# Kernel optimization log

Measured on AMD Instinct MI355X. Metric: run time of the kernel, lower is better.

The kernel has to match this reference:

```python
import jax, jax.numpy as jnp
import numpy as np

N_NODES = 100000
IN_CH, HID_CH, OUT_CH = 128, 256, 128
N_EDGES = 1600000


def setup_inputs() -> dict:
    key = jax.random.key(0)
    ks = jax.random.split(key, 12)
    x = jax.random.normal(ks[0], (N_NODES, IN_CH), dtype=jnp.float32)
    edge_index = jax.random.randint(ks[1], (2, N_EDGES), 0, N_NODES, dtype=jnp.int32)
    s1 = 1.0 / np.sqrt(IN_CH)
    s2 = 1.0 / np.sqrt(HID_CH)
    return {
        "x": x,
        "edge_index": edge_index,
        "eps1": jnp.zeros((), jnp.float32),
        "W1a": jax.random.uniform(ks[2], (IN_CH, HID_CH), jnp.float32, -s1, s1),
        "b1a": jax.random.uniform(ks[3], (HID_CH,), jnp.float32, -s1, s1),
        "W1b": jax.random.uniform(ks[4], (HID_CH, HID_CH), jnp.float32, -s2, s2),
        "b1b": jax.random.uniform(ks[5], (HID_CH,), jnp.float32, -s2, s2),
        "eps2": jnp.zeros((), jnp.float32),
        "W2a": jax.random.uniform(ks[6], (HID_CH, HID_CH), jnp.float32, -s2, s2),
        "b2a": jax.random.uniform(ks[7], (HID_CH,), jnp.float32, -s2, s2),
        "W2b": jax.random.uniform(ks[8], (HID_CH, OUT_CH), jnp.float32, -s2, s2),
        "b2b": jax.random.uniform(ks[9], (OUT_CH,), jnp.float32, -s2, s2),
    }


def _gin_conv(x, src, dst, eps, Wa, ba, Wb, bb):
    # sum-aggregate source features into destinations: [N, d]
    agg = jax.ops.segment_sum(x[src], dst, num_segments=N_NODES)
    h = (1.0 + eps) * x + agg
    h = jax.nn.relu(h @ Wa + ba)
    return h @ Wb + bb


def reference(x, edge_index, eps1, W1a, b1a, W1b, b1b, eps2, W2a, b2a, W2b, b2b):
    src, dst = edge_index[0], edge_index[1]
    h = _gin_conv(x, src, dst, eps1, W1a, b1a, W1b, b1b)
    h = jax.nn.relu(h)
    out = _gin_conv(h, src, dst, eps2, W2a, b2a, W2b, b2b)
    return out
```

## Files before the change

### kernel.cpp

```cpp
#include <hip/hip_runtime.h>

#define N_NODES 100000
#define N_EDGES 1600000
#define NB 782
#define SC_BLK 256

typedef __attribute__((ext_vector_type(8))) short short8;
typedef __attribute__((ext_vector_type(4))) float float4e;

#define GLDS16(g, l)                                                   \
  __builtin_amdgcn_global_load_lds(                                    \
      (const __attribute__((address_space(1))) unsigned int*)(g),      \
      (__attribute__((address_space(3))) unsigned int*)(l), 16, 0, 0)

__device__ __forceinline__ unsigned short f2bf(float f) {
  unsigned u = __float_as_uint(f);
  u += 0x7FFFu + ((u >> 16) & 1u);
  return (unsigned short)(u >> 16);
}
__device__ __forceinline__ float bf2f(unsigned short h) {
  return __uint_as_float(((unsigned)h) << 16);
}

__global__ __launch_bounds__(256) void histA_k(const int* __restrict__ dst,
                                               int* __restrict__ bh, int nE) {
  __shared__ int h[NB];
  const int blk = blockIdx.x, tid = threadIdx.x;
  for (int b = tid; b < NB; b += 256) h[b] = 0;
  __syncthreads();
  const int epb = (nE + SC_BLK - 1) / SC_BLK;
  const int i1 = min(blk * epb + epb, nE);
  for (int i = blk * epb + tid; i < i1; i += 256)
    atomicAdd(&h[dst[i] >> 7], 1);
  __syncthreads();
  for (int b = tid; b < NB; b += 256) bh[b * SC_BLK + blk] = h[b];
}

__global__ __launch_bounds__(256) void scanW_k(int* __restrict__ bh,
                                               int* __restrict__ tot) {
  const int b = blockIdx.x * 4 + (threadIdx.x >> 6);
  const int lane = threadIdx.x & 63;
  if (b >= NB) return;
  const int base = b * SC_BLK + lane * 4;
  int v[4];
#pragma unroll
  for (int j = 0; j < 4; ++j) v[j] = bh[base + j];
  int ls = v[0] + v[1] + v[2] + v[3];
  int x = ls;
  for (int off = 1; off < 64; off <<= 1) {
    int y = __shfl_up(x, off);
    if (lane >= off) x += y;
  }
  int run = x - ls;
#pragma unroll
  for (int j = 0; j < 4; ++j) {
    int t = v[j];
    bh[base + j] = run;
    run += t;
  }
  if (lane == 63) tot[b] = run;
}

__global__ __launch_bounds__(1024) void scanB2_k(const int* __restrict__ tot,
                                                 int* __restrict__ bucketStart) {
  __shared__ int sm[1024];
  const int tid = threadIdx.x;
  int v = (tid < NB) ? tot[tid] : 0;
  sm[tid] = v;
  __syncthreads();
  for (int off = 1; off < 1024; off <<= 1) {
    int t = (tid >= off) ? sm[tid - off] : 0;
    __syncthreads();
    sm[tid] += t;
    __syncthreads();
  }
  if (tid < NB) bucketStart[tid] = sm[tid] - v;
  if (tid == NB - 1) bucketStart[NB] = sm[tid];
}

__global__ __launch_bounds__(256) void scatter2_k(
    const int* __restrict__ src, const int* __restrict__ dst,
    const int* __restrict__ bucketStart, const int* __restrict__ bh,
    unsigned int* __restrict__ packed, int nE) {
  __shared__ int cur[NB];
  const int blk = blockIdx.x, tid = threadIdx.x;
  for (int b = tid; b < NB; b += 256)
    cur[b] = bucketStart[b] + bh[b * SC_BLK + blk];
  __syncthreads();
  const int epb = (nE + SC_BLK - 1) / SC_BLK;
  const int i1 = min(blk * epb + epb, nE);
  for (int i = blk * epb + tid; i < i1; i += 256) {
    int d = dst[i];
    int s = src[i];
    int p = atomicAdd(&cur[d >> 7], 1);
    packed[p] = ((unsigned)s << 7) | (unsigned)(d & 127);
  }
}

__global__ __launch_bounds__(256) void fillB_k(
    const int* __restrict__ bucketStart, const unsigned int* __restrict__ packed,
    int* __restrict__ rowEnd, int* __restrict__ sortedSrc, int nNodes) {
  __shared__ int cnt[128];
  __shared__ int cur[128];
  const int b = blockIdx.x;
  const int tid = threadIdx.x;
  const int s0 = bucketStart[b];
  const int ne = bucketStart[b + 1] - s0;
  if (tid < 128) cnt[tid] = 0;
  __syncthreads();
  for (int i = tid; i < ne; i += 256)
    atomicAdd(&cnt[packed[s0 + i] & 127u], 1);
  __syncthreads();
  int v = (tid < 128) ? cnt[tid] : 0;
  for (int off = 1; off < 128; off <<= 1) {
    int t = (tid < 128 && tid >= off) ? cnt[tid - off] : 0;
    __syncthreads();
    if (tid < 128) cnt[tid] += t;
    __syncthreads();
  }
  if (tid < 128) {
    cur[tid] = s0 + cnt[tid] - v;
    int node = b * 128 + tid;
    if (node < nNodes) rowEnd[node] = s0 + cnt[tid];
  }
  __syncthreads();
  for (int i = tid; i < ne; i += 256) {
    unsigned p = packed[s0 + i];
    int idx = atomicAdd(&cur[p & 127u], 1);
    sortedSrc[idx] = (int)(p >> 7);
  }
}

__global__ __launch_bounds__(256) void wprep_k(
    const float* __restrict__ W, unsigned short* __restrict__ th,
    unsigned short* __restrict__ tl, int K, int N) {
  int i = blockIdx.x * blockDim.x + threadIdx.x;
  if (i < K * N) {
    int k = i / N, n = i % N;
    float v = W[i];
    unsigned short h = f2bf(v);
    unsigned short l = f2bf(v - bf2f(h));
    th[(long)n * K + k] = h;
    tl[(long)n * K + k] = l;
  }
}

__global__ __launch_bounds__(256) void xprep_k(const float* __restrict__ x,
                                               unsigned short* __restrict__ xh,
                                               int n) {
  int i = blockIdx.x * blockDim.x + threadIdx.x;
  if (i < n) xh[i] = f2bf(x[i]);
}

template <bool XF32>
__global__ __launch_bounds__(256) void agg_s_k(
    const unsigned short* __restrict__ feat_h, const float* __restrict__ xf,
    const unsigned short* __restrict__ xh, const unsigned short* __restrict__ xl,
    const float* __restrict__ epsp, const int* __restrict__ rowEnd,
    const int* __restrict__ sortedSrc, unsigned short* __restrict__ oh,
    unsigned short* __restrict__ ol, int M, int S, int off) {
  constexpr int V = 2;
  const int lane = threadIdx.x & 63;
  const int w = (int)((blockIdx.x * blockDim.x + threadIdx.x) >> 6);
  if (w >= M) return;
  const int start = w ? rowEnd[w - 1] : 0;
  const int end = rowEnd[w];
  const int c0 = lane * V + off;

  float acc[V] = {};
  int e = start;
  for (; e + 8 <= end; e += 8) {
    int si[8];
#pragma unroll
    for (int q = 0; q < 8; ++q) si[q] = sortedSrc[e + q];
    ushort2 t[8];
#pragma unroll
    for (int q = 0; q < 8; ++q)
      t[q] = *(const ushort2*)(feat_h + (long)si[q] * S + c0);
#pragma unroll
    for (int q = 0; q < 8; ++q) {
      acc[0] += bf2f(t[q].x);
      acc[1] += bf2f(t[q].y);
    }
  }
  for (; e + 4 <= end; e += 4) {
    int s0 = sortedSrc[e + 0];
    int s1 = sortedSrc[e + 1];
    int s2 = sortedSrc[e + 2];
    int s3 = sortedSrc[e + 3];
    ushort2 a = *(const ushort2*)(feat_h + (long)s0 * S + c0);
    ushort2 b = *(const ushort2*)(feat_h + (long)s1 * S + c0);
    ushort2 c = *(const ushort2*)(feat_h + (long)s2 * S + c0);
    ushort2 d = *(const ushort2*)(feat_h + (long)s3 * S + c0);
    acc[0] += bf2f(a.x) + bf2f(b.x) + bf2f(c.x) + bf2f(d.x);
    acc[1] += bf2f(a.y) + bf2f(b.y) + bf2f(c.y) + bf2f(d.y);
  }
  for (; e < end; ++e) {
    ushort2 a = *(const ushort2*)(feat_h + (long)sortedSrc[e] * S + c0);
    acc[0] += bf2f(a.x);
    acc[1] += bf2f(a.y);
  }

  const float s = 1.0f + epsp[0];
  float xv[V];
  if constexpr (XF32) {
#pragma unroll
    for (int v = 0; v < V; ++v) xv[v] = xf[(long)w * S + c0 + v];
  } else {
#pragma unroll
    for (int v = 0; v < V; ++v)
      xv[v] = bf2f(xh[(long)w * S + c0 + v]) + bf2f(xl[(long)w * S + c0 + v]);
  }

  unsigned short hv[V], lv[V];
#pragma unroll
  for (int v = 0; v < V; ++v) {
    float res = fmaf(s, xv[v], acc[v]);
    hv[v] = f2bf(res);
    lv[v] = f2bf(res - bf2f(hv[v]));
  }
  *(ushort2*)&oh[(long)w * S + c0] = make_ushort2(hv[0], hv[1]);
  *(ushort2*)&ol[(long)w * S + c0] = make_ushort2(lv[0], lv[1]);
}

__device__ __forceinline__ short8 lds_rd(const unsigned short* base, int r,
                                         int q) {
  int L = r * 64 + q * 16;
  int P = L ^ (((L >> 7) & 7) << 4);
  return *(const short8*)((const char*)base + P);
}

#define MFMA_BF16 __builtin_amdgcn_mfma_f32_16x16x32_bf16

template <int NY, bool RELU, bool HILO>
__global__ __launch_bounds__(256, 2) void gemm128_k(
    const unsigned short* __restrict__ Ah, const unsigned short* __restrict__ Al,
    const unsigned short* __restrict__ Bth, const unsigned short* __restrict__ Btl,
    const float* __restrict__ bias, float* __restrict__ outf,
    unsigned short* __restrict__ oh, unsigned short* __restrict__ ol,
    int M, int K, int NOUT) {
  __shared__ unsigned short Sm[16384];
  unsigned short* Ash = Sm;
  unsigned short* Asl = Sm + 4096;
  unsigned short* Bsh = Sm + 8192;
  unsigned short* Bsl = Sm + 12288;

  const int tid = threadIdx.x;
  const int lane = tid & 63;
  const int wave = tid >> 6;
  const int l15 = lane & 15;
  const int quad = lane >> 4;
  const int wm = wave >> 1;
  const int wn = wave & 1;

  const int nwg = gridDim.x;
  const int q8 = nwg >> 3, r8 = nwg & 7;
  const int xcd = blockIdx.x & 7, idx = blockIdx.x >> 3;
  const int lin =
      (xcd < r8 ? xcd * (q8 + 1) : r8 * (q8 + 1) + (xcd - r8) * q8) + idx;
  int bx, n0;
  if (NY == 2) {
    bx = lin >> 1;
    n0 = (lin & 1) * 128;
  } else {
    bx = lin;
    n0 = 0;
  }
  const int m0 = bx * 128;

  float4e acc[4][4];
#pragma unroll
  for (int i = 0; i < 4; ++i)
#pragma unroll
    for (int j = 0; j < 4; ++j) acc[i][j] = 0.0f;

  for (int k0 = 0; k0 < K; k0 += 32) {
#pragma unroll
    for (int h = 0; h < 2; ++h) {
      int c = h * 256 + tid;
      int P = c * 16;
      int L = P ^ (((P >> 7) & 7) << 4);
      int r = L >> 6;
      int q = (L >> 4) & 3;
      int ra = min(m0 + r, M - 1);
      long ga = (long)ra * K + k0 + q * 8;
      GLDS16(Ah + ga, &Ash[c * 8]);
      GLDS16(Al + ga, &Asl[c * 8]);
      long gb = (long)(n0 + r) * K + k0 + q * 8;
      GLDS16(Bth + gb, &Bsh[c * 8]);
      GLDS16(Btl + gb, &Bsl[c * 8]);
    }
    __syncthreads();

    short8 ah[4], al[4];
#pragma unroll
    for (int mi = 0; mi < 4; ++mi) {
      ah[mi] = lds_rd(Ash, wm * 64 + mi * 16 + l15, quad);
      al[mi] = lds_rd(Asl, wm * 64 + mi * 16 + l15, quad);
    }
#pragma unroll
    for (int ni = 0; ni < 4; ++ni) {
      short8 bh = lds_rd(Bsh, wn * 64 + ni * 16 + l15, quad);
      short8 bl = lds_rd(Bsl, wn * 64 + ni * 16 + l15, quad);
#pragma unroll
      for (int mi = 0; mi < 4; ++mi) {
        acc[mi][ni] = MFMA_BF16(ah[mi], bh, acc[mi][ni], 0, 0, 0);
        acc[mi][ni] = MFMA_BF16(ah[mi], bl, acc[mi][ni], 0, 0, 0);
        acc[mi][ni] = MFMA_BF16(al[mi], bh, acc[mi][ni], 0, 0, 0);
      }
    }
    __syncthreads();
  }

  if constexpr (HILO) {
#pragma unroll
    for (int pass = 0; pass < 2; ++pass) {
#pragma unroll
      for (int ni = 0; ni < 4; ++ni) {
        int col = wn * 64 + ni * 16 + l15;
        float bj = bias[n0 + col];
#pragma unroll
        for (int mi = 0; mi < 4; ++mi) {
#pragma unroll
          for (int r = 0; r < 4; ++r) {
            int row = wm * 64 + mi * 16 + quad * 4 + r;
            float v = acc[mi][ni][r] + bj;
            if constexpr (RELU) v = fmaxf(v, 0.0f);
            unsigned short hv = f2bf(v);
            unsigned short wv = pass ? f2bf(v - bf2f(hv)) : hv;
            int B = row * 256 + col * 2;
            int SB = B ^ (((row >> 2) & 3) << 5);
            *(unsigned short*)((char*)Sm + SB) = wv;
          }
        }
      }
      __syncthreads();
      unsigned short* dst = pass ? ol : oh;
#pragma unroll
      for (int i = 0; i < 8; ++i) {
        int li = i * 256 + tid;
        int row = li >> 4, chk = li & 15;
        int B = row * 256 + chk * 16;
        int SB = B ^ (((row >> 2) & 3) << 5);
        if (m0 + row < M)
          *(short8*)&dst[(long)(m0 + row) * NOUT + n0 + chk * 8] =
              *(const short8*)((const char*)Sm + SB);
      }
      __syncthreads();
    }
  } else {
#pragma unroll
    for (int ni = 0; ni < 4; ++ni) {
      int col = n0 + wn * 64 + ni * 16 + l15;
      float bj = bias[col];
#pragma unroll
      for (int mi = 0; mi < 4; ++mi) {
        int rbase = m0 + wm * 64 + mi * 16 + quad * 4;
#pragma unroll
        for (int r = 0; r < 4; ++r) {
          int row = rbase + r;
          if (row < M) {
            float v = acc[mi][ni][r] + bj;
            if constexpr (RELU) v = fmaxf(v, 0.0f);
            outf[(long)row * NOUT + col] = v;
          }
        }
      }
    }
  }
}

extern "C" void kernel_launch(void* const* d_in, const int* in_sizes, int n_in,
                              void* d_out, int out_size, void* d_ws, size_t ws_size,
                              hipStream_t stream) {
  const float* x    = (const float*)d_in[0];
  const int*   ei   = (const int*)d_in[1];
  const float* eps1 = (const float*)d_in[2];
  const float* W1a  = (const float*)d_in[3];
  const float* b1a  = (const float*)d_in[4];
  const float* W1b  = (const float*)d_in[5];
  const float* b1b  = (const float*)d_in[6];
  const float* eps2 = (const float*)d_in[7];
  const float* W2a  = (const float*)d_in[8];
  const float* b2a  = (const float*)d_in[9];
  const float* W2b  = (const float*)d_in[10];
  const float* b2b  = (const float*)d_in[11];
  float* out = (float*)d_out;

  const int* srcp = ei;
  const int* dstp = ei + N_EDGES;

  char* ws = (char*)d_ws;
  const size_t SZ = (size_t)N_NODES * 256 * sizeof(float);
  char* P1 = ws;
  char* P2 = ws + SZ;

  unsigned short* C1h = (unsigned short*)P1;
  unsigned short* C1l = C1h + (size_t)N_NODES * 128;
  unsigned short* xh  = C1l + (size_t)N_NODES * 128;
  unsigned short* T1h = (unsigned short*)P2;
  unsigned short* T1l = T1h + (size_t)N_NODES * 256;
  unsigned short* Hh = (unsigned short*)P1;
  unsigned short* Hl = Hh + (size_t)N_NODES * 256;
  unsigned short* C2h = (unsigned short*)P2;
  unsigned short* C2l = C2h + (size_t)N_NODES * 256;
  unsigned short* T2h = (unsigned short*)P1;
  unsigned short* T2l = T2h + (size_t)N_NODES * 256;
  unsigned short* W2bh = (unsigned short*)P2;
  unsigned short* W2bl = W2bh + 128 * 256;

  char* ob = (char*)d_out;
  int* rowEnd    = (int*)(ob + 400 * 1024);
  int* sortedSrc = (int*)(ob + 800 * 1024);
  size_t wofs = 7340032;
  unsigned short* W1ah = (unsigned short*)(ob + wofs);
  unsigned short* W1al = W1ah + 256 * 128;
  unsigned short* W1bh = (unsigned short*)(ob + wofs + 2 * 65536);
  unsigned short* W1bl = W1bh + 256 * 256;
  unsigned short* W2ah = (unsigned short*)(ob + wofs + 2 * 65536 + 2 * 131072);
  unsigned short* W2al = W2ah + 256 * 256;
  unsigned int* packed = (unsigned int*)(ob + 16 * 1024 * 1024);
  int* bucketStart = (int*)(ob + 28 * 1024 * 1024);
  int* bucketTot   = (int*)(ob + 28 * 1024 * 1024 + 8192);
  int* blockHist   = (int*)(ob + 30 * 1024 * 1024);

  dim3 blk(256);
  dim3 gAgg((N_NODES + 3) / 4);
  dim3 gW1((128 * 256 + 255) / 256);
  dim3 gW2((256 * 256 + 255) / 256);
  dim3 gXp((N_NODES * 128 + 255) / 256);
  dim3 gGemm2(((N_NODES + 127) / 128) * 2);
  dim3 gGemm1((N_NODES + 127) / 128);

  histA_k<<<dim3(SC_BLK), blk, 0, stream>>>(dstp, blockHist, N_EDGES);
  scanW_k<<<dim3((NB + 3) / 4), blk, 0, stream>>>(blockHist, bucketTot);
  scanB2_k<<<1, dim3(1024), 0, stream>>>(bucketTot, bucketStart);
  scatter2_k<<<dim3(SC_BLK), blk, 0, stream>>>(srcp, dstp, bucketStart,
                                               blockHist, packed, N_EDGES);
  fillB_k<<<dim3(NB), blk, 0, stream>>>(bucketStart, packed, rowEnd, sortedSrc,
                                        N_NODES);
  xprep_k<<<gXp, blk, 0, stream>>>(x, xh, N_NODES * 128);
  wprep_k<<<gW1, blk, 0, stream>>>(W1a, W1ah, W1al, 128, 256);
  wprep_k<<<gW2, blk, 0, stream>>>(W1b, W1bh, W1bl, 256, 256);
  wprep_k<<<gW2, blk, 0, stream>>>(W2a, W2ah, W2al, 256, 256);

  agg_s_k<true><<<gAgg, blk, 0, stream>>>(
      xh, x, nullptr, nullptr, eps1, rowEnd, sortedSrc, C1h, C1l, N_NODES, 128, 0);
  gemm128_k<2, true, true><<<gGemm2, blk, 0, stream>>>(
      C1h, C1l, W1ah, W1al, b1a, nullptr, T1h, T1l, N_NODES, 128, 256);
  gemm128_k<2, true, true><<<gGemm2, blk, 0, stream>>>(
      T1h, T1l, W1bh, W1bl, b1b, nullptr, Hh, Hl, N_NODES, 256, 256);

  agg_s_k<false><<<gAgg, blk, 0, stream>>>(
      Hh, nullptr, Hh, Hl, eps2, rowEnd, sortedSrc, C2h, C2l, N_NODES, 256, 0);
  agg_s_k<false><<<gAgg, blk, 0, stream>>>(
      Hh, nullptr, Hh, Hl, eps2, rowEnd, sortedSrc, C2h, C2l, N_NODES, 256, 128);
  gemm128_k<2, true, true><<<gGemm2, blk, 0, stream>>>(
      C2h, C2l, W2ah, W2al, b2a, nullptr, T2h, T2l, N_NODES, 256, 256);
  wprep_k<<<gW1, blk, 0, stream>>>(W2b, W2bh, W2bl, 256, 128);
  gemm128_k<1, false, false><<<gGemm1, blk, 0, stream>>>(
      T2h, T2l, W2bh, W2bl, b2b, out, nullptr, nullptr, N_NODES, 256, 128);
}
```

Measured before the change: 616.4 us.

## Merge layer-2 aggregation halves and deepen GEMM K-tile to 64

The two half-width aggregation launches for the 256-channel layer become one kernel in which each lane gathers four bf16 values per source row, and a 16-edge unrolled gather loop is added. The GEMM K-step goes from 32 to 64 with a 64 KB shared-memory tile and an adjusted swizzle. This halves the number of barriers and K-loop iterations, and the layer-2 sortedSrc index list is read once instead of twice. The larger LDS footprint may limit occupancy below the requested 2 blocks per SM, and the wider unrolls raise register pressure.

```diff
diff --git a/kernel.cpp b/kernel.cpp
--- a/kernel.cpp
+++ b/kernel.cpp
@@ -152,64 +152,100 @@
   if (i < n) xh[i] = f2bf(x[i]);
 }
 
-template <bool XF32>
-__global__ __launch_bounds__(256) void agg_s_k(
+template <int C, bool XF32>
+__global__ __launch_bounds__(256) void agg_k(
     const unsigned short* __restrict__ feat_h, const float* __restrict__ xf,
     const unsigned short* __restrict__ xh, const unsigned short* __restrict__ xl,
     const float* __restrict__ epsp, const int* __restrict__ rowEnd,
     const int* __restrict__ sortedSrc, unsigned short* __restrict__ oh,
-    unsigned short* __restrict__ ol, int M, int S, int off) {
-  constexpr int V = 2;
+    unsigned short* __restrict__ ol, int M) {
+  constexpr int V = C / 64;
   const int lane = threadIdx.x & 63;
   const int w = (int)((blockIdx.x * blockDim.x + threadIdx.x) >> 6);
   if (w >= M) return;
   const int start = w ? rowEnd[w - 1] : 0;
   const int end = rowEnd[w];
-  const int c0 = lane * V + off;
+  const int c0 = lane * V;
 
   float acc[V] = {};
   int e = start;
+  for (; e + 16 <= end; e += 16) {
+    int si[16];
+#pragma unroll
+    for (int q = 0; q < 16; ++q) si[q] = sortedSrc[e + q];
+    if constexpr (V == 4) {
+      ushort4 t[16];
+#pragma unroll
+      for (int q = 0; q < 16; ++q)
+        t[q] = *(const ushort4*)(feat_h + (long)si[q] * C + c0);
+#pragma unroll
+      for (int q = 0; q < 16; ++q) {
+        acc[0] += bf2f(t[q].x);
+        acc[1] += bf2f(t[q].y);
+        acc[2] += bf2f(t[q].z);
+        acc[3] += bf2f(t[q].w);
+      }
+    } else {
+      ushort2 t[16];
+#pragma unroll
+      for (int q = 0; q < 16; ++q)
+        t[q] = *(const ushort2*)(feat_h + (long)si[q] * C + c0);
+#pragma unroll
+      for (int q = 0; q < 16; ++q) {
+        acc[0] += bf2f(t[q].x);
+        acc[1] += bf2f(t[q].y);
+      }
+    }
+  }
   for (; e + 8 <= end; e += 8) {
     int si[8];
 #pragma unroll
     for (int q = 0; q < 8; ++q) si[q] = sortedSrc[e + q];
-    ushort2 t[8];
-#pragma unroll
-    for (int q = 0; q < 8; ++q)
-      t[q] = *(const ushort2*)(feat_h + (long)si[q] * S + c0);
-#pragma unroll
-    for (int q = 0; q < 8; ++q) {
-      acc[0] += bf2f(t[q].x);
-      acc[1] += bf2f(t[q].y);
-    }
-  }
-  for (; e + 4 <= end; e += 4) {
-    int s0 = sortedSrc[e + 0];
-    int s1 = sortedSrc[e + 1];
-    int s2 = sortedSrc[e + 2];
-    int s3 = sortedSrc[e + 3];
-    ushort2 a = *(const ushort2*)(feat_h + (long)s0 * S + c0);
-    ushort2 b = *(const ushort2*)(feat_h + (long)s1 * S + c0);
-    ushort2 c = *(const ushort2*)(feat_h + (long)s2 * S + c0);
-    ushort2 d = *(const ushort2*)(feat_h + (long)s3 * S + c0);
-    acc[0] += bf2f(a.x) + bf2f(b.x) + bf2f(c.x) + bf2f(d.x);
-    acc[1] += bf2f(a.y) + bf2f(b.y) + bf2f(c.y) + bf2f(d.y);
+    if constexpr (V == 4) {
+      ushort4 t[8];
+#pragma unroll
+      for (int q = 0; q < 8; ++q)
+        t[q] = *(const ushort4*)(feat_h + (long)si[q] * C + c0);
+#pragma unroll
+      for (int q = 0; q < 8; ++q) {
+        acc[0] += bf2f(t[q].x);
+        acc[1] += bf2f(t[q].y);
+        acc[2] += bf2f(t[q].z);
+        acc[3] += bf2f(t[q].w);
+      }
+    } else {
+      ushort2 t[8];
+#pragma unroll
+      for (int q = 0; q < 8; ++q)
+        t[q] = *(const ushort2*)(feat_h + (long)si[q] * C + c0);
+#pragma unroll
+      for (int q = 0; q < 8; ++q) {
+        acc[0] += bf2f(t[q].x);
+        acc[1] += bf2f(t[q].y);
+      }
+    }
   }
   for (; e < end; ++e) {
-    ushort2 a = *(const ushort2*)(feat_h + (long)sortedSrc[e] * S + c0);
-    acc[0] += bf2f(a.x);
-    acc[1] += bf2f(a.y);
+    const unsigned short* r = feat_h + (long)sortedSrc[e] * C + c0;
+    if constexpr (V == 4) {
+      ushort4 a = *(const ushort4*)r;
+      acc[0] += bf2f(a.x); acc[1] += bf2f(a.y);
+      acc[2] += bf2f(a.z); acc[3] += bf2f(a.w);
+    } else {
+      ushort2 a = *(const ushort2*)r;
+      acc[0] += bf2f(a.x); acc[1] += bf2f(a.y);
+    }
   }
 
   const float s = 1.0f + epsp[0];
   float xv[V];
   if constexpr (XF32) {
 #pragma unroll
-    for (int v = 0; v < V; ++v) xv[v] = xf[(long)w * S + c0 + v];
+    for (int v = 0; v < V; ++v) xv[v] = xf[(long)w * C + c0 + v];
   } else {
 #pragma unroll
     for (int v = 0; v < V; ++v)
-      xv[v] = bf2f(xh[(long)w * S + c0 + v]) + bf2f(xl[(long)w * S + c0 + v]);
+      xv[v] = bf2f(xh[(long)w * C + c0 + v]) + bf2f(xl[(long)w * C + c0 + v]);
   }
 
   unsigned short hv[V], lv[V];
@@ -219,13 +255,18 @@
     hv[v] = f2bf(res);
     lv[v] = f2bf(res - bf2f(hv[v]));
   }
-  *(ushort2*)&oh[(long)w * S + c0] = make_ushort2(hv[0], hv[1]);
-  *(ushort2*)&ol[(long)w * S + c0] = make_ushort2(lv[0], lv[1]);
-}
-
-__device__ __forceinline__ short8 lds_rd(const unsigned short* base, int r,
-                                         int q) {
-  int L = r * 64 + q * 16;
+  if constexpr (V == 4) {
+    *(ushort4*)&oh[(long)w * C + c0] = make_ushort4(hv[0], hv[1], hv[2], hv[3]);
+    *(ushort4*)&ol[(long)w * C + c0] = make_ushort4(lv[0], lv[1], lv[2], lv[3]);
+  } else {
+    *(ushort2*)&oh[(long)w * C + c0] = make_ushort2(hv[0], hv[1]);
+    *(ushort2*)&ol[(long)w * C + c0] = make_ushort2(lv[0], lv[1]);
+  }
+}
+
+__device__ __forceinline__ short8 lds_rd64(const unsigned short* base, int r,
+                                           int c16) {
+  int L = r * 128 + c16 * 16;
   int P = L ^ (((L >> 7) & 7) << 4);
   return *(const short8*)((const char*)base + P);
 }
@@ -239,11 +280,11 @@
     const float* __restrict__ bias, float* __restrict__ outf,
     unsigned short* __restrict__ oh, unsigned short* __restrict__ ol,
     int M, int K, int NOUT) {
-  __shared__ unsigned short Sm[16384];
-  unsigned short* Ash = Sm;
-  unsigned short* Asl = Sm + 4096;
-  unsigned short* Bsh = Sm + 8192;
-  unsigned short* Bsl = Sm + 12288;
+  __shared__ char smem[65536];
+  unsigned short* Ash = (unsigned short*)smem;
+  unsigned short* Asl = (unsigned short*)(smem + 16384);
+  unsigned short* Bsh = (unsigned short*)(smem + 32768);
+  unsigned short* Bsl = (unsigned short*)(smem + 49152);
 
   const int tid = threadIdx.x;
   const int lane = tid & 63;
@@ -274,14 +315,14 @@
 #pragma unroll
     for (int j = 0; j < 4; ++j) acc[i][j] = 0.0f;
 
-  for (int k0 = 0; k0 < K; k0 += 32) {
-#pragma unroll
-    for (int h = 0; h < 2; ++h) {
+  for (int k0 = 0; k0 < K; k0 += 64) {
+#pragma unroll
+    for (int h = 0; h < 4; ++h) {
       int c = h * 256 + tid;
       int P = c * 16;
       int L = P ^ (((P >> 7) & 7) << 4);
-      int r = L >> 6;
-      int q = (L >> 4) & 3;
+      int r = L >> 7;
+      int q = (L >> 4) & 7;
       int ra = min(m0 + r, M - 1);
       long ga = (long)ra * K + k0 + q * 8;
       GLDS16(Ah + ga, &Ash[c * 8]);
@@ -292,21 +333,24 @@
     }
     __syncthreads();
 
-    short8 ah[4], al[4];
-#pragma unroll
-    for (int mi = 0; mi < 4; ++mi) {
-      ah[mi] = lds_rd(Ash, wm * 64 + mi * 16 + l15, quad);
-      al[mi] = lds_rd(Asl, wm * 64 + mi * 16 + l15, quad);
-    }
-#pragma unroll
-    for (int ni = 0; ni < 4; ++ni) {
-      short8 bh = lds_rd(Bsh, wn * 64 + ni * 16 + l15, quad);
-      short8 bl = lds_rd(Bsl, wn * 64 + ni * 16 + l15, quad);
+#pragma unroll
+    for (int hh = 0; hh < 2; ++hh) {
+      short8 ah[4], al[4];
 #pragma unroll
       for (int mi = 0; mi < 4; ++mi) {
-        acc[mi][ni] = MFMA_BF16(ah[mi], bh, acc[mi][ni], 0, 0, 0);
-        acc[mi][ni] = MFMA_BF16(ah[mi], bl, acc[mi][ni], 0, 0, 0);
-        acc[mi][ni] = MFMA_BF16(al[mi], bh, acc[mi][ni], 0, 0, 0);
+        ah[mi] = lds_rd64(Ash, wm * 64 + mi * 16 + l15, hh * 4 + quad);
+        al[mi] = lds_rd64(Asl, wm * 64 + mi * 16 + l15, hh * 4 + quad);
+      }
+#pragma unroll
+      for (int ni = 0; ni < 4; ++ni) {
+        short8 bh = lds_rd64(Bsh, wn * 64 + ni * 16 + l15, hh * 4 + quad);
+        short8 bl = lds_rd64(Bsl, wn * 64 + ni * 16 + l15, hh * 4 + quad);
+#pragma unroll
+        for (int mi = 0; mi < 4; ++mi) {
+          acc[mi][ni] = MFMA_BF16(ah[mi], bh, acc[mi][ni], 0, 0, 0);
+          acc[mi][ni] = MFMA_BF16(ah[mi], bl, acc[mi][ni], 0, 0, 0);
+          acc[mi][ni] = MFMA_BF16(al[mi], bh, acc[mi][ni], 0, 0, 0);
+        }
       }
     }
     __syncthreads();
@@ -330,7 +374,7 @@
             unsigned short wv = pass ? f2bf(v - bf2f(hv)) : hv;
             int B = row * 256 + col * 2;
             int SB = B ^ (((row >> 2) & 3) << 5);
-            *(unsigned short*)((char*)Sm + SB) = wv;
+            *(unsigned short*)(smem + SB) = wv;
           }
         }
       }
@@ -344,7 +388,7 @@
         int SB = B ^ (((row >> 2) & 3) << 5);
         if (m0 + row < M)
           *(short8*)&dst[(long)(m0 + row) * NOUT + n0 + chk * 8] =
-              *(const short8*)((const char*)Sm + SB);
+              *(const short8*)(smem + SB);
       }
       __syncthreads();
     }
@@ -444,17 +488,15 @@
   wprep_k<<<gW2, blk, 0, stream>>>(W1b, W1bh, W1bl, 256, 256);
   wprep_k<<<gW2, blk, 0, stream>>>(W2a, W2ah, W2al, 256, 256);
 
-  agg_s_k<true><<<gAgg, blk, 0, stream>>>(
-      xh, x, nullptr, nullptr, eps1, rowEnd, sortedSrc, C1h, C1l, N_NODES, 128, 0);
+  agg_k<128, true><<<gAgg, blk, 0, stream>>>(
+      xh, x, nullptr, nullptr, eps1, rowEnd, sortedSrc, C1h, C1l, N_NODES);
   gemm128_k<2, true, true><<<gGemm2, blk, 0, stream>>>(
       C1h, C1l, W1ah, W1al, b1a, nullptr, T1h, T1l, N_NODES, 128, 256);
   gemm128_k<2, true, true><<<gGemm2, blk, 0, stream>>>(
       T1h, T1l, W1bh, W1bl, b1b, nullptr, Hh, Hl, N_NODES, 256, 256);
 
-  agg_s_k<false><<<gAgg, blk, 0, stream>>>(
-      Hh, nullptr, Hh, Hl, eps2, rowEnd, sortedSrc, C2h, C2l, N_NODES, 256, 0);
-  agg_s_k<false><<<gAgg, blk, 0, stream>>>(
-      Hh, nullptr, Hh, Hl, eps2, rowEnd, sortedSrc, C2h, C2l, N_NODES, 256, 128);
+  agg_k<256, false><<<gAgg, blk, 0, stream>>>(
+      Hh, nullptr, Hh, Hl, eps2, rowEnd, sortedSrc, C2h, C2l, N_NODES);
   gemm128_k<2, true, true><<<gGemm2, blk, 0, stream>>>(
       C2h, C2l, W2ah, W2al, b2a, nullptr, T2h, T2l, N_NODES, 256, 256);
   wprep_k<<<gW1, blk, 0, stream>>>(W2b, W2bh, W2bl, 256, 128);
```

After: 637.8 us. 1.03x slower.
